# Kernel tuning notes

Measured on AMD Instinct MI355X. Metric: run time of the kernel, lower is better.

Reference implementation:

```python
import jax, jax.numpy as jnp
import numpy as np

N = 50000      # nodes
E = 800000     # edges
IN = 128       # in_channels
H = 128        # hidden_channels
OUT = 40       # out_channels (classes)
EPS = 1e-5     # LayerNorm eps


def _glorot(key, fan_in, fan_out):
    lim = np.sqrt(6.0 / (fan_in + fan_out)).astype(np.float32)
    return jax.random.uniform(key, (fan_in, fan_out), jnp.float32, -lim, lim)


def setup_inputs() -> dict:
    key = jax.random.key(0)
    ks = jax.random.split(key, 8)
    x = jax.random.normal(ks[0], (N, IN), jnp.float32)
    edge_index = jax.random.randint(ks[1], (2, E), 0, N, jnp.int32)
    return {
        "x": x,
        "W0": _glorot(ks[2], IN, H), "b0": jnp.zeros((H,), jnp.float32),
        "W1": _glorot(ks[3], H, H),  "b1": jnp.zeros((H,), jnp.float32),
        "W2": _glorot(ks[4], H, OUT), "b2": jnp.zeros((OUT,), jnp.float32),
        "ln1_g": jnp.ones((H,), jnp.float32), "ln1_b": jnp.zeros((H,), jnp.float32),
        "ln2_g": jnp.ones((H,), jnp.float32), "ln2_b": jnp.zeros((H,), jnp.float32),
        "edge_index": edge_index,
    }


def reference(x, W0, b0, W1, b1, W2, b2, ln1_g, ln1_b, ln2_g, ln2_b, edge_index):
    # GCN normalization with self-loops: A_hat = D^-1/2 (A + I) D^-1/2
    self_idx = jnp.arange(N, dtype=edge_index.dtype)
    src = jnp.concatenate([edge_index[0], self_idx])  # [E+N]
    dst = jnp.concatenate([edge_index[1], self_idx])
    deg = jax.ops.segment_sum(jnp.ones_like(src, jnp.float32), dst, num_segments=N)
    dinv = jax.lax.rsqrt(deg)  # deg >= 1 thanks to self-loops
    norm = dinv[src] * dinv[dst]  # [E+N]

    def conv(h, W, b):
        h = h @ W                                  # [N, F] dense GEMM
        msg = h[src] * norm[:, None]               # gather + scale [E+N, F]
        return jax.ops.segment_sum(msg, dst, num_segments=N) + b

    def layernorm(h, g, b):
        mu = jnp.mean(h, axis=-1, keepdims=True)
        var = jnp.mean(jnp.square(h - mu), axis=-1, keepdims=True)
        return (h - mu) * jax.lax.rsqrt(var + EPS) * g + b

    # layer 0 (note: original uses lns[i+1], so lns[0] is never applied)
    h = jax.nn.relu(layernorm(conv(x, W0, b0), ln1_g, ln1_b))
    # dropout is identity in eval mode
    h = jax.nn.relu(layernorm(conv(h, W1, b1), ln2_g, ln2_b))
    h = conv(h, W2, b2)
    return jax.nn.log_softmax(h, axis=-1)
```

## Files before the change

### kernel.cpp

```cpp
#include <hip/hip_runtime.h>
#include <math.h>

typedef __attribute__((ext_vector_type(8))) short bf16x8;
typedef __attribute__((ext_vector_type(4))) float f32x4;
typedef unsigned short u16;
typedef unsigned int u32;

static __device__ __forceinline__ u16 f2bf(float f) {
    unsigned u = __float_as_uint(f);
    unsigned r = (u + 0x7fff + ((u >> 16) & 1)) >> 16;
    return (u16)r;
}
static __device__ __forceinline__ float bf2f(u16 h) {
    return __uint_as_float(((unsigned)h) << 16);
}
static __device__ __forceinline__ float pk_lo(u32 u) { return __uint_as_float(u << 16); }
static __device__ __forceinline__ float pk_hi(u32 u) { return __uint_as_float(u & 0xffff0000u); }

__global__ void init_k(int* __restrict__ counts, int n, int gN,
                       const float* __restrict__ W0, const float* __restrict__ W1,
                       const float* __restrict__ W2,
                       u16* __restrict__ w0hi, u16* __restrict__ w0lo,
                       u16* __restrict__ w1hi, u16* __restrict__ w1lo,
                       u16* __restrict__ w2hi, u16* __restrict__ w2lo) {
    int b = blockIdx.x;
    if (b < gN) {
        int i = b * 256 + threadIdx.x;
        if (i < n) counts[i] = 0;
        return;
    }
    int i = (b - gN) * 256 + threadIdx.x;
    const float* W; u16 *hi, *lo; int COLS, cin, idx;
    if (i < 16384)      { W = W0; hi = w0hi; lo = w0lo; COLS = 128; cin = 128; idx = i; }
    else if (i < 32768) { W = W1; hi = w1hi; lo = w1lo; COLS = 128; cin = 128; idx = i - 16384; }
    else if (i < 40960) { W = W2; hi = w2hi; lo = w2lo; COLS = 64;  cin = 40;  idx = i - 32768; }
    else return;
    int k = idx / COLS, col = idx % COLS;
    float v = (col < cin) ? W[k * cin + col] : 0.f;
    u16 h = f2bf(v);
    u16 l = f2bf(v - bf2f(h));
    int ct = col >> 4, ks = k >> 5, ln = (col & 15) + (((k >> 3) & 3) << 4), j = k & 7;
    int pos = (((ct * 4 + ks) * 64 + ln) << 3) + j;
    hi[pos] = h; lo[pos] = l;
}

__global__ void count_rank_k(const int* __restrict__ dst, int* __restrict__ counts,
                             u16* __restrict__ rank, int e) {
    int i = blockIdx.x * 256 + threadIdx.x;
    if (i < e) rank[i] = (u16)atomicAdd(&counts[dst[i]], 1);
}
__global__ __launch_bounds__(1024) void scan1_k(const int* __restrict__ counts,
                                                int* __restrict__ offs,
                                                int* __restrict__ bsum,
                                                float* __restrict__ dinv, int n) {
    __shared__ int ws[16];
    int tid = threadIdx.x;
    int i = blockIdx.x * 1024 + tid;
    int lane = tid & 63, w = tid >> 6;
    int c = (i < n) ? counts[i] : 0;
    if (i < n) dinv[i] = rsqrtf((float)c + 1.0f);
    int s = c;
#pragma unroll
    for (int o = 1; o < 64; o <<= 1) { int t = __shfl_up(s, o); if (lane >= o) s += t; }
    if (lane == 63) ws[w] = s;
    __syncthreads();
    if (w == 0) {
        int x = (lane < 16) ? ws[lane] : 0;
#pragma unroll
        for (int o = 1; o < 16; o <<= 1) { int t = __shfl_up(x, o); if (lane >= o) x += t; }
        if (lane < 16) ws[lane] = x;
    }
    __syncthreads();
    int base = (w > 0) ? ws[w - 1] : 0;
    int incl = base + s;
    if (i < n) offs[i + 1] = incl;
    if (tid == 1023) bsum[blockIdx.x] = incl;
}
__global__ void scan23_k(int* __restrict__ offs, const int* __restrict__ bsum,
                         int nb, int n) {
    __shared__ int pre[64];
    int tid = threadIdx.x;
    if (tid < 64) {
        int v = (tid < nb) ? bsum[tid] : 0;
#pragma unroll
        for (int o = 1; o < 64; o <<= 1) { int t = __shfl_up(v, o); if (tid >= o) v += t; }
        pre[tid] = v;
    }
    __syncthreads();
    int i = blockIdx.x * 256 + tid;
    if (i == 0) offs[0] = 0;
    if (i < n) {
        int b = i >> 10;
        offs[i + 1] += (b > 0) ? pre[b - 1] : 0;
    }
}

__global__ __launch_bounds__(256) void fill_gemm1_k(const int* __restrict__ src,
                                                    const int* __restrict__ dst,
                                                    const u16* __restrict__ rank,
                                                    const int* __restrict__ offs,
                                                    u16* __restrict__ csr, int e, int fillBlocks,
                                                    const float* __restrict__ A,
                                                    const u16* __restrict__ Whi,
                                                    const u16* __restrict__ Wlo,
                                                    const float* __restrict__ dinv,
                                                    u16* __restrict__ C, int nrows) {
    if ((int)blockIdx.x < fillBlocks) {
        int i = blockIdx.x * 256 + threadIdx.x;
        if (i < e) csr[offs[dst[i]] + (int)rank[i]] = (u16)src[i];
        return;
    }
    constexpr int COLS = 128;
    int bid = blockIdx.x - fillBlocks;
    int wave = threadIdx.x >> 6, lane = threadIdx.x & 63;
    int r0 = bid * 64 + wave * 16;
    int arow = min(r0 + (lane & 15), nrows - 1);
    int kbase = (lane >> 4) * 8;

    bf16x8 ahi[4], alo[4];
#pragma unroll
    for (int ks = 0; ks < 4; ++ks) {
        const float* ap = &A[(long)arow * 128 + ks * 32 + kbase];
        float4 f0 = *(const float4*)ap;
        float4 f1 = *(const float4*)(ap + 4);
        float fv[8] = {f0.x, f0.y, f0.z, f0.w, f1.x, f1.y, f1.z, f1.w};
#pragma unroll
        for (int j = 0; j < 8; ++j) {
            u16 h = f2bf(fv[j]);
            ahi[ks][j] = (short)h;
            alo[ks][j] = (short)f2bf(fv[j] - bf2f(h));
        }
    }
    float dscale[4];
#pragma unroll
    for (int r = 0; r < 4; ++r) {
        int orow = r0 + (lane >> 4) * 4 + r;
        dscale[r] = (orow < nrows) ? dinv[orow] : 0.f;
    }
#pragma unroll
    for (int ct = 0; ct < COLS / 16; ct += 2) {
        f32x4 acc0 = {0.f, 0.f, 0.f, 0.f}, acc1 = {0.f, 0.f, 0.f, 0.f};
#pragma unroll
        for (int ks = 0; ks < 4; ++ks) {
            int fo0 = ((ct * 4 + ks) * 64 + lane) * 8;
            int fo1 = (((ct + 1) * 4 + ks) * 64 + lane) * 8;
            bf16x8 bhi0 = *(const bf16x8*)&Whi[fo0];
            bf16x8 blo0 = *(const bf16x8*)&Wlo[fo0];
            bf16x8 bhi1 = *(const bf16x8*)&Whi[fo1];
            bf16x8 blo1 = *(const bf16x8*)&Wlo[fo1];
            acc0 = __builtin_amdgcn_mfma_f32_16x16x32_bf16(ahi[ks], bhi0, acc0, 0, 0, 0);
            acc1 = __builtin_amdgcn_mfma_f32_16x16x32_bf16(ahi[ks], bhi1, acc1, 0, 0, 0);
            acc0 = __builtin_amdgcn_mfma_f32_16x16x32_bf16(alo[ks], bhi0, acc0, 0, 0, 0);
            acc1 = __builtin_amdgcn_mfma_f32_16x16x32_bf16(alo[ks], bhi1, acc1, 0, 0, 0);
            acc0 = __builtin_amdgcn_mfma_f32_16x16x32_bf16(ahi[ks], blo0, acc0, 0, 0, 0);
            acc1 = __builtin_amdgcn_mfma_f32_16x16x32_bf16(ahi[ks], blo1, acc1, 0, 0, 0);
        }
#pragma unroll
        for (int r = 0; r < 4; ++r) {
            int orow = r0 + (lane >> 4) * 4 + r;
            if (orow < nrows) {
                C[(long)orow * COLS + ct * 16 + (lane & 15)] = f2bf(acc0[r] * dscale[r]);
                C[(long)orow * COLS + (ct + 1) * 16 + (lane & 15)] = f2bf(acc1[r] * dscale[r]);
            }
        }
    }
}

template<int COLS>
__global__ __launch_bounds__(256) void mfma_gemm_bf16a_k(const u16* __restrict__ A,
                                                         const u16* __restrict__ Whi,
                                                         const u16* __restrict__ Wlo,
                                                         const float* __restrict__ dinv,
                                                         u16* __restrict__ C, int nrows) {
    int wave = threadIdx.x >> 6, lane = threadIdx.x & 63;
    int r0 = blockIdx.x * 64 + wave * 16;
    int arow = min(r0 + (lane & 15), nrows - 1);
    int kbase = (lane >> 4) * 8;

    bf16x8 a[4];
#pragma unroll
    for (int ks = 0; ks < 4; ++ks)
        a[ks] = *(const bf16x8*)&A[(long)arow * 128 + ks * 32 + kbase];

    float dscale[4];
#pragma unroll
    for (int r = 0; r < 4; ++r) {
        int orow = r0 + (lane >> 4) * 4 + r;
        dscale[r] = (orow < nrows) ? dinv[orow] : 0.f;
    }
#pragma unroll
    for (int ct = 0; ct < COLS / 16; ct += 2) {
        f32x4 acc0 = {0.f, 0.f, 0.f, 0.f}, acc1 = {0.f, 0.f, 0.f, 0.f};
#pragma unroll
        for (int ks = 0; ks < 4; ++ks) {
            int fo0 = ((ct * 4 + ks) * 64 + lane) * 8;
            int fo1 = (((ct + 1) * 4 + ks) * 64 + lane) * 8;
            bf16x8 bhi0 = *(const bf16x8*)&Whi[fo0];
            bf16x8 blo0 = *(const bf16x8*)&Wlo[fo0];
            bf16x8 bhi1 = *(const bf16x8*)&Whi[fo1];
            bf16x8 blo1 = *(const bf16x8*)&Wlo[fo1];
            acc0 = __builtin_amdgcn_mfma_f32_16x16x32_bf16(a[ks], bhi0, acc0, 0, 0, 0);
            acc1 = __builtin_amdgcn_mfma_f32_16x16x32_bf16(a[ks], bhi1, acc1, 0, 0, 0);
            acc0 = __builtin_amdgcn_mfma_f32_16x16x32_bf16(a[ks], blo0, acc0, 0, 0, 0);
            acc1 = __builtin_amdgcn_mfma_f32_16x16x32_bf16(a[ks], blo1, acc1, 0, 0, 0);
        }
#pragma unroll
        for (int r = 0; r < 4; ++r) {
            int orow = r0 + (lane >> 4) * 4 + r;
            if (orow < nrows) {
                C[(long)orow * COLS + ct * 16 + (lane & 15)] = f2bf(acc0[r] * dscale[r]);
                C[(long)orow * COLS + (ct + 1) * 16 + (lane & 15)] = f2bf(acc1[r] * dscale[r]);
            }
        }
    }
}

__global__ __launch_bounds__(256) void agg_ln_relu_k(const u16* __restrict__ Cs,
                                                     const int* __restrict__ offs,
                                                     const u16* __restrict__ csr,
                                                     const float* __restrict__ dinv,
                                                     const float* __restrict__ bias,
                                                     const float* __restrict__ g,
                                                     const float* __restrict__ b,
                                                     u16* __restrict__ out, int n) {
    int wid = (blockIdx.x * 256 + threadIdx.x) >> 6;
    int lane = threadIdx.x & 63;
    if (wid >= n) return;
    const u32* C2 = (const u32*)Cs;
    u32 su = C2[(long)wid * 64 + lane];
    float ax = pk_lo(su), ay = pk_hi(su), bx2 = 0.f, by2 = 0.f;
    int beg = offs[wid], end = offs[wid + 1];
    int j = beg;
    while (j < end) {
        int take = min(64, end - j);
        int myidx = (lane < take) ? (int)csr[j + lane] : 0;
        int k = 0;
        for (; k + 8 <= take; k += 8) {
            int i0 = __shfl(myidx, k),     i1 = __shfl(myidx, k + 1);
            int i2 = __shfl(myidx, k + 2), i3 = __shfl(myidx, k + 3);
            int i4 = __shfl(myidx, k + 4), i5 = __shfl(myidx, k + 5);
            int i6 = __shfl(myidx, k + 6), i7 = __shfl(myidx, k + 7);
            u32 u0 = C2[(long)i0 * 64 + lane], u1 = C2[(long)i1 * 64 + lane];
            u32 u2 = C2[(long)i2 * 64 + lane], u3 = C2[(long)i3 * 64 + lane];
            u32 u4 = C2[(long)i4 * 64 + lane], u5 = C2[(long)i5 * 64 + lane];
            u32 u6 = C2[(long)i6 * 64 + lane], u7 = C2[(long)i7 * 64 + lane];
            ax += pk_lo(u0) + pk_lo(u1) + pk_lo(u2) + pk_lo(u3);
            ay += pk_hi(u0) + pk_hi(u1) + pk_hi(u2) + pk_hi(u3);
            bx2 += pk_lo(u4) + pk_lo(u5) + pk_lo(u6) + pk_lo(u7);
            by2 += pk_hi(u4) + pk_hi(u5) + pk_hi(u6) + pk_hi(u7);
        }
        for (; k < take; ++k) {
            int i0 = __shfl(myidx, k);
            u32 u0 = C2[(long)i0 * 64 + lane];
            ax += pk_lo(u0); ay += pk_hi(u0);
        }
        j += take;
    }
    float w = dinv[wid];
    float2 bia = ((const float2*)bias)[lane];
    float t0 = (ax + bx2) * w + bia.x;
    float t1 = (ay + by2) * w + bia.y;
    float s = t0 + t1;
#pragma unroll
    for (int off = 32; off; off >>= 1) s += __shfl_xor(s, off);
    float mu = s * (1.f / 128.f);
    float d0 = t0 - mu, d1 = t1 - mu;
    float v = d0 * d0 + d1 * d1;
#pragma unroll
    for (int off = 32; off; off >>= 1) v += __shfl_xor(v, off);
    float rstd = rsqrtf(v * (1.f / 128.f) + 1e-5f);
    float2 gv = ((const float2*)g)[lane];
    float2 bv = ((const float2*)b)[lane];
    float y0 = fmaxf(0.f, d0 * rstd * gv.x + bv.x);
    float y1 = fmaxf(0.f, d1 * rstd * gv.y + bv.y);
    ((u32*)out)[(long)wid * 64 + lane] = ((u32)f2bf(y1) << 16) | f2bf(y0);
}

__global__ __launch_bounds__(256) void agg_lsm_k(const u16* __restrict__ Cs,
                                                 const int* __restrict__ offs,
                                                 const u16* __restrict__ csr,
                                                 const float* __restrict__ dinv,
                                                 const float* __restrict__ b2,
                                                 float* __restrict__ out, int n) {
    int wid = (blockIdx.x * 256 + threadIdx.x) >> 6;
    int lane = threadIdx.x & 63;
    if (wid >= n) return;
    float aa = bf2f(Cs[(long)wid * 64 + lane]), ab = 0.f;
    int beg = offs[wid], end = offs[wid + 1];
    int j = beg;
    while (j < end) {
        int take = min(64, end - j);
        int myidx = (lane < take) ? (int)csr[j + lane] : 0;
        int k = 0;
        for (; k + 8 <= take; k += 8) {
            int i0 = __shfl(myidx, k),     i1 = __shfl(myidx, k + 1);
            int i2 = __shfl(myidx, k + 2), i3 = __shfl(myidx, k + 3);
            int i4 = __shfl(myidx, k + 4), i5 = __shfl(myidx, k + 5);
            int i6 = __shfl(myidx, k + 6), i7 = __shfl(myidx, k + 7);
            float v0 = bf2f(Cs[(long)i0 * 64 + lane]), v1 = bf2f(Cs[(long)i1 * 64 + lane]);
            float v2 = bf2f(Cs[(long)i2 * 64 + lane]), v3 = bf2f(Cs[(long)i3 * 64 + lane]);
            float v4 = bf2f(Cs[(long)i4 * 64 + lane]), v5 = bf2f(Cs[(long)i5 * 64 + lane]);
            float v6 = bf2f(Cs[(long)i6 * 64 + lane]), v7 = bf2f(Cs[(long)i7 * 64 + lane]);
            aa += v0 + v1 + v2 + v3;
            ab += v4 + v5 + v6 + v7;
        }
        for (; k < take; ++k) {
            int i0 = __shfl(myidx, k);
            aa += bf2f(Cs[(long)i0 * 64 + lane]);
        }
        j += take;
    }
    float v = (lane < 40) ? (aa + ab) * dinv[wid] + b2[lane] : -INFINITY;
    float m = v;
#pragma unroll
    for (int off = 32; off; off >>= 1) m = fmaxf(m, __shfl_xor(m, off));
    float e = (lane < 40) ? expf(v - m) : 0.f;
    float s = e;
#pragma unroll
    for (int off = 32; off; off >>= 1) s += __shfl_xor(s, off);
    float r = v - m - logf(s);
    if (lane < 40) out[(long)wid * 40 + lane] = r;
}

extern "C" void kernel_launch(void* const* d_in, const int* in_sizes, int n_in,
                              void* d_out, int out_size, void* d_ws, size_t ws_size,
                              hipStream_t stream) {
    const float* x    = (const float*)d_in[0];
    const float* W0   = (const float*)d_in[1];
    const float* b0   = (const float*)d_in[2];
    const float* W1   = (const float*)d_in[3];
    const float* b1   = (const float*)d_in[4];
    const float* W2   = (const float*)d_in[5];
    const float* b2   = (const float*)d_in[6];
    const float* ln1g = (const float*)d_in[7];
    const float* ln1b = (const float*)d_in[8];
    const float* ln2g = (const float*)d_in[9];
    const float* ln2b = (const float*)d_in[10];
    const int*   ei   = (const int*)d_in[11];

    const int N = in_sizes[0] / 128;
    const int E = in_sizes[11] / 2;
    const int* esrc = ei;
    const int* edst = ei + E;
    float* out = (float*)d_out;

    const int Npad = ((N + 255) / 256) * 256;

    int* counts  = (int*)d_ws;
    int* offs    = counts + Npad;
    int* bsum    = offs + Npad;
    u16* rank16  = (u16*)(bsum + 64);
    u16* csr16   = rank16 + E;
    float* dinv  = (float*)(csr16 + E);
    u16* bufA    = (u16*)(dinv + Npad);
    u16* bufB    = bufA + (size_t)N * 128;
    u16* w0hi    = bufB + (size_t)N * 128;
    u16* w0lo    = w0hi + 16384;
    u16* w1hi    = w0lo + 16384;
    u16* w1lo    = w1hi + 16384;
    u16* w2hi    = w1lo + 16384;
    u16* w2lo    = w2hi + 8192;

    dim3 blk(256);
    int gN = (N + 255) / 256, gE = (E + 255) / 256;
    int nb1024 = (N + 1023) / 1024;
    int gG = (N + 63) / 64;
    int gW = (N + 3) / 4;

    init_k<<<gN + 160, blk, 0, stream>>>(counts, N, gN, W0, W1, W2,
                                         w0hi, w0lo, w1hi, w1lo, w2hi, w2lo);
    count_rank_k<<<gE, blk, 0, stream>>>(edst, counts, rank16, E);
    scan1_k<<<nb1024, 1024, 0, stream>>>(counts, offs, bsum, dinv, N);
    scan23_k<<<gN, blk, 0, stream>>>(offs, bsum, nb1024, N);
    fill_gemm1_k<<<gE + gG, blk, 0, stream>>>(esrc, edst, rank16, offs, csr16, E, gE,
                                              x, w0hi, w0lo, dinv, bufA, N);
    agg_ln_relu_k<<<gW, blk, 0, stream>>>(bufA, offs, csr16, dinv, b0, ln1g, ln1b, bufB, N);
    mfma_gemm_bf16a_k<128><<<gG, blk, 0, stream>>>(bufB, w1hi, w1lo, dinv, bufA, N);
    agg_ln_relu_k<<<gW, blk, 0, stream>>>(bufA, offs, csr16, dinv, b1, ln2g, ln2b, bufB, N);
    mfma_gemm_bf16a_k<64><<<gG, blk, 0, stream>>>(bufB, w2hi, w2lo, dinv, bufA, N);
    agg_lsm_k<<<gW, blk, 0, stream>>>(bufA, offs, csr16, dinv, b2, out, N);
}
```

Baseline: 207.1 us.

## Split wavefront across multiple edges per iteration with vectorized row loads in aggregation

After: 211.7 us. 1.02x slower.

```diff
diff --git a/kernel.cpp b/kernel.cpp
--- a/kernel.cpp
+++ b/kernel.cpp
@@ -227,53 +227,66 @@
     int lane = threadIdx.x & 63;
     if (wid >= n) return;
     const u32* C2 = (const u32*)Cs;
-    u32 su = C2[(long)wid * 64 + lane];
-    float ax = pk_lo(su), ay = pk_hi(su), bx2 = 0.f, by2 = 0.f;
+    int half = lane >> 5;
+    int w = lane & 31;
+    float a0 = 0.f, a1 = 0.f, a2 = 0.f, a3 = 0.f;
+    float c0 = 0.f, c1 = 0.f, c2 = 0.f, c3 = 0.f;
+    if (half == 0) {
+        uint2 u = *(const uint2*)&C2[(size_t)wid * 64 + 2 * w];
+        a0 = pk_lo(u.x); a1 = pk_hi(u.x); a2 = pk_lo(u.y); a3 = pk_hi(u.y);
+    }
     int beg = offs[wid], end = offs[wid + 1];
-    int j = beg;
-    while (j < end) {
+    for (int j = beg; j < end; j += 64) {
         int take = min(64, end - j);
         int myidx = (lane < take) ? (int)csr[j + lane] : 0;
         int k = 0;
-        for (; k + 8 <= take; k += 8) {
-            int i0 = __shfl(myidx, k),     i1 = __shfl(myidx, k + 1);
-            int i2 = __shfl(myidx, k + 2), i3 = __shfl(myidx, k + 3);
-            int i4 = __shfl(myidx, k + 4), i5 = __shfl(myidx, k + 5);
-            int i6 = __shfl(myidx, k + 6), i7 = __shfl(myidx, k + 7);
-            u32 u0 = C2[(long)i0 * 64 + lane], u1 = C2[(long)i1 * 64 + lane];
-            u32 u2 = C2[(long)i2 * 64 + lane], u3 = C2[(long)i3 * 64 + lane];
-            u32 u4 = C2[(long)i4 * 64 + lane], u5 = C2[(long)i5 * 64 + lane];
-            u32 u6 = C2[(long)i6 * 64 + lane], u7 = C2[(long)i7 * 64 + lane];
-            ax += pk_lo(u0) + pk_lo(u1) + pk_lo(u2) + pk_lo(u3);
-            ay += pk_hi(u0) + pk_hi(u1) + pk_hi(u2) + pk_hi(u3);
-            bx2 += pk_lo(u4) + pk_lo(u5) + pk_lo(u6) + pk_lo(u7);
-            by2 += pk_hi(u4) + pk_hi(u5) + pk_hi(u6) + pk_hi(u7);
-        }
-        for (; k < take; ++k) {
-            int i0 = __shfl(myidx, k);
-            u32 u0 = C2[(long)i0 * 64 + lane];
-            ax += pk_lo(u0); ay += pk_hi(u0);
-        }
-        j += take;
-    }
-    float w = dinv[wid];
-    float2 bia = ((const float2*)bias)[lane];
-    float t0 = (ax + bx2) * w + bia.x;
-    float t1 = (ay + by2) * w + bia.y;
-    float s = t0 + t1;
-#pragma unroll
-    for (int off = 32; off; off >>= 1) s += __shfl_xor(s, off);
-    float mu = s * (1.f / 128.f);
-    float d0 = t0 - mu, d1 = t1 - mu;
-    float v = d0 * d0 + d1 * d1;
-#pragma unroll
-    for (int off = 32; off; off >>= 1) v += __shfl_xor(v, off);
-    float rstd = rsqrtf(v * (1.f / 128.f) + 1e-5f);
-    float2 gv = ((const float2*)g)[lane];
-    float2 bv = ((const float2*)b)[lane];
+        for (; k + 16 <= take; k += 16) {
+#pragma unroll
+            for (int it = 0; it < 8; ++it) {
+                int s = __shfl(myidx, k + it * 2 + half);
+                uint2 u = *(const uint2*)&C2[(size_t)s * 64 + 2 * w];
+                if (it & 1) { c0 += pk_lo(u.x); c1 += pk_hi(u.x); c2 += pk_lo(u.y); c3 += pk_hi(u.y); }
+                else        { a0 += pk_lo(u.x); a1 += pk_hi(u.x); a2 += pk_lo(u.y); a3 += pk_hi(u.y); }
+            }
+        }
+        for (; k < take; k += 2) {
+            int e = k + half;
+            bool v = e < take;
+            int s = __shfl(myidx, v ? e : 0);
+            if (v) {
+                uint2 u = *(const uint2*)&C2[(size_t)s * 64 + 2 * w];
+                a0 += pk_lo(u.x); a1 += pk_hi(u.x); a2 += pk_lo(u.y); a3 += pk_hi(u.y);
+            }
+        }
+    }
+    a0 += c0; a1 += c1; a2 += c2; a3 += c3;
+    a0 += __shfl_xor(a0, 32); a1 += __shfl_xor(a1, 32);
+    a2 += __shfl_xor(a2, 32); a3 += __shfl_xor(a3, 32);
+    float dv = dinv[wid];
+    float4 bi = ((const float4*)bias)[w];
+    float t0 = a0 * dv + bi.x, t1 = a1 * dv + bi.y;
+    float t2 = a2 * dv + bi.z, t3 = a3 * dv + bi.w;
+    float s4 = t0 + t1 + t2 + t3;
+#pragma unroll
+    for (int o = 1; o < 32; o <<= 1) s4 += __shfl_xor(s4, o);
+    float mu = s4 * (1.f / 128.f);
+    float d0 = t0 - mu, d1 = t1 - mu, d2 = t2 - mu, d3 = t3 - mu;
+    float q = d0 * d0 + d1 * d1 + d2 * d2 + d3 * d3;
+#pragma unroll
+    for (int o = 1; o < 32; o <<= 1) q += __shfl_xor(q, o);
+    float rstd = rsqrtf(q * (1.f / 128.f) + 1e-5f);
+    float4 gv = ((const float4*)g)[w];
+    float4 bv = ((const float4*)b)[w];
     float y0 = fmaxf(0.f, d0 * rstd * gv.x + bv.x);
     float y1 = fmaxf(0.f, d1 * rstd * gv.y + bv.y);
-    ((u32*)out)[(long)wid * 64 + lane] = ((u32)f2bf(y1) << 16) | f2bf(y0);
+    float y2 = fmaxf(0.f, d2 * rstd * gv.z + bv.z);
+    float y3 = fmaxf(0.f, d3 * rstd * gv.w + bv.w);
+    if (half == 0) {
+        uint2 o2;
+        o2.x = ((u32)f2bf(y1) << 16) | f2bf(y0);
+        o2.y = ((u32)f2bf(y3) << 16) | f2bf(y2);
+        *(uint2*)&((u32*)out)[(size_t)wid * 64 + 2 * w] = o2;
+    }
 }
 
 __global__ __launch_bounds__(256) void agg_lsm_k(const u16* __restrict__ Cs,
@@ -285,41 +298,64 @@
     int wid = (blockIdx.x * 256 + threadIdx.x) >> 6;
     int lane = threadIdx.x & 63;
     if (wid >= n) return;
-    float aa = bf2f(Cs[(long)wid * 64 + lane]), ab = 0.f;
+    const u32* C2 = (const u32*)Cs;
+    int slot = lane >> 4;
+    int w = lane & 15;
+    float a0 = 0.f, a1 = 0.f, a2 = 0.f, a3 = 0.f;
+    float c0 = 0.f, c1 = 0.f, c2 = 0.f, c3 = 0.f;
+    if (slot == 0) {
+        uint2 u = *(const uint2*)&C2[(size_t)wid * 32 + 2 * w];
+        a0 = pk_lo(u.x); a1 = pk_hi(u.x); a2 = pk_lo(u.y); a3 = pk_hi(u.y);
+    }
     int beg = offs[wid], end = offs[wid + 1];
-    int j = beg;
-    while (j < end) {
+    for (int j = beg; j < end; j += 64) {
         int take = min(64, end - j);
         int myidx = (lane < take) ? (int)csr[j + lane] : 0;
         int k = 0;
-        for (; k + 8 <= take; k += 8) {
-            int i0 = __shfl(myidx, k),     i1 = __shfl(myidx, k + 1);
-            int i2 = __shfl(myidx, k + 2), i3 = __shfl(myidx, k + 3);
-            int i4 = __shfl(myidx, k + 4), i5 = __shfl(myidx, k + 5);
-            int i6 = __shfl(myidx, k + 6), i7 = __shfl(myidx, k + 7);
-            float v0 = bf2f(Cs[(long)i0 * 64 + lane]), v1 = bf2f(Cs[(long)i1 * 64 + lane]);
-            float v2 = bf2f(Cs[(long)i2 * 64 + lane]), v3 = bf2f(Cs[(long)i3 * 64 + lane]);
-            float v4 = bf2f(Cs[(long)i4 * 64 + lane]), v5 = bf2f(Cs[(long)i5 * 64 + lane]);
-            float v6 = bf2f(Cs[(long)i6 * 64 + lane]), v7 = bf2f(Cs[(long)i7 * 64 + lane]);
-            aa += v0 + v1 + v2 + v3;
-            ab += v4 + v5 + v6 + v7;
-        }
-        for (; k < take; ++k) {
-            int i0 = __shfl(myidx, k);
-            aa += bf2f(Cs[(long)i0 * 64 + lane]);
-        }
-        j += take;
-    }
-    float v = (lane < 40) ? (aa + ab) * dinv[wid] + b2[lane] : -INFINITY;
-    float m = v;
-#pragma unroll
-    for (int off = 32; off; off >>= 1) m = fmaxf(m, __shfl_xor(m, off));
-    float e = (lane < 40) ? expf(v - m) : 0.f;
-    float s = e;
-#pragma unroll
-    for (int off = 32; off; off >>= 1) s += __shfl_xor(s, off);
-    float r = v - m - logf(s);
-    if (lane < 40) out[(long)wid * 40 + lane] = r;
+        for (; k + 16 <= take; k += 16) {
+#pragma unroll
+            for (int it = 0; it < 4; ++it) {
+                int s = __shfl(myidx, k + it * 4 + slot);
+                uint2 u = *(const uint2*)&C2[(size_t)s * 32 + 2 * w];
+                if (it & 1) { c0 += pk_lo(u.x); c1 += pk_hi(u.x); c2 += pk_lo(u.y); c3 += pk_hi(u.y); }
+                else        { a0 += pk_lo(u.x); a1 += pk_hi(u.x); a2 += pk_lo(u.y); a3 += pk_hi(u.y); }
+            }
+        }
+        for (; k < take; k += 4) {
+            int e = k + slot;
+            bool v = e < take;
+            int s = __shfl(myidx, v ? e : 0);
+            if (v) {
+                uint2 u = *(const uint2*)&C2[(size_t)s * 32 + 2 * w];
+                a0 += pk_lo(u.x); a1 += pk_hi(u.x); a2 += pk_lo(u.y); a3 += pk_hi(u.y);
+            }
+        }
+    }
+    a0 += c0; a1 += c1; a2 += c2; a3 += c3;
+#pragma unroll
+    for (int m2 = 16; m2 < 64; m2 <<= 1) {
+        a0 += __shfl_xor(a0, m2); a1 += __shfl_xor(a1, m2);
+        a2 += __shfl_xor(a2, m2); a3 += __shfl_xor(a3, m2);
+    }
+    float dv = dinv[wid];
+    float v0 = -INFINITY, v1 = -INFINITY, v2 = -INFINITY, v3 = -INFINITY;
+    if (w < 10) {
+        float4 bb = ((const float4*)b2)[w];
+        v0 = a0 * dv + bb.x; v1 = a1 * dv + bb.y;
+        v2 = a2 * dv + bb.z; v3 = a3 * dv + bb.w;
+    }
+    float m = fmaxf(fmaxf(v0, v1), fmaxf(v2, v3));
+#pragma unroll
+    for (int o = 1; o < 16; o <<= 1) m = fmaxf(m, __shfl_xor(m, o));
+    float es = 0.f;
+    if (w < 10) es = expf(v0 - m) + expf(v1 - m) + expf(v2 - m) + expf(v3 - m);
+#pragma unroll
+    for (int o = 1; o < 16; o <<= 1) es += __shfl_xor(es, o);
+    float ls = logf(es);
+    if (slot == 0 && w < 10) {
+        float4 r = make_float4(v0 - m - ls, v1 - m - ls, v2 - m - ls, v3 - m - ls);
+        *(float4*)&out[(size_t)wid * 40 + 4 * w] = r;
+    }
 }
 
 extern "C" void kernel_launch(void* const* d_in, const int* in_sizes, int n_in,
```

## Overlap GEMM with edge counting and split aggregation/GEMM into node halves

Applied to the files above, without the earlier changes.

After: 205.7 us, median of 2. About the same (-0.7%).

```diff
diff --git a/kernel.cpp b/kernel.cpp
--- a/kernel.cpp
+++ b/kernel.cpp
@@ -44,74 +44,11 @@
     hi[pos] = h; lo[pos] = l;
 }
 
-__global__ void count_rank_k(const int* __restrict__ dst, int* __restrict__ counts,
-                             u16* __restrict__ rank, int e) {
-    int i = blockIdx.x * 256 + threadIdx.x;
-    if (i < e) rank[i] = (u16)atomicAdd(&counts[dst[i]], 1);
-}
-__global__ __launch_bounds__(1024) void scan1_k(const int* __restrict__ counts,
-                                                int* __restrict__ offs,
-                                                int* __restrict__ bsum,
-                                                float* __restrict__ dinv, int n) {
-    __shared__ int ws[16];
-    int tid = threadIdx.x;
-    int i = blockIdx.x * 1024 + tid;
-    int lane = tid & 63, w = tid >> 6;
-    int c = (i < n) ? counts[i] : 0;
-    if (i < n) dinv[i] = rsqrtf((float)c + 1.0f);
-    int s = c;
-#pragma unroll
-    for (int o = 1; o < 64; o <<= 1) { int t = __shfl_up(s, o); if (lane >= o) s += t; }
-    if (lane == 63) ws[w] = s;
-    __syncthreads();
-    if (w == 0) {
-        int x = (lane < 16) ? ws[lane] : 0;
-#pragma unroll
-        for (int o = 1; o < 16; o <<= 1) { int t = __shfl_up(x, o); if (lane >= o) x += t; }
-        if (lane < 16) ws[lane] = x;
-    }
-    __syncthreads();
-    int base = (w > 0) ? ws[w - 1] : 0;
-    int incl = base + s;
-    if (i < n) offs[i + 1] = incl;
-    if (tid == 1023) bsum[blockIdx.x] = incl;
-}
-__global__ void scan23_k(int* __restrict__ offs, const int* __restrict__ bsum,
-                         int nb, int n) {
-    __shared__ int pre[64];
-    int tid = threadIdx.x;
-    if (tid < 64) {
-        int v = (tid < nb) ? bsum[tid] : 0;
-#pragma unroll
-        for (int o = 1; o < 64; o <<= 1) { int t = __shfl_up(v, o); if (tid >= o) v += t; }
-        pre[tid] = v;
-    }
-    __syncthreads();
-    int i = blockIdx.x * 256 + tid;
-    if (i == 0) offs[0] = 0;
-    if (i < n) {
-        int b = i >> 10;
-        offs[i + 1] += (b > 0) ? pre[b - 1] : 0;
-    }
-}
-
-__global__ __launch_bounds__(256) void fill_gemm1_k(const int* __restrict__ src,
-                                                    const int* __restrict__ dst,
-                                                    const u16* __restrict__ rank,
-                                                    const int* __restrict__ offs,
-                                                    u16* __restrict__ csr, int e, int fillBlocks,
-                                                    const float* __restrict__ A,
-                                                    const u16* __restrict__ Whi,
-                                                    const u16* __restrict__ Wlo,
-                                                    const float* __restrict__ dinv,
-                                                    u16* __restrict__ C, int nrows) {
-    if ((int)blockIdx.x < fillBlocks) {
-        int i = blockIdx.x * 256 + threadIdx.x;
-        if (i < e) csr[offs[dst[i]] + (int)rank[i]] = (u16)src[i];
-        return;
-    }
+static __device__ __forceinline__ void gemm1_body(int bid, const float* __restrict__ A,
+                                                  const u16* __restrict__ Whi,
+                                                  const u16* __restrict__ Wlo,
+                                                  u16* __restrict__ C, int nrows) {
     constexpr int COLS = 128;
-    int bid = blockIdx.x - fillBlocks;
     int wave = threadIdx.x >> 6, lane = threadIdx.x & 63;
     int r0 = bid * 64 + wave * 16;
     int arow = min(r0 + (lane & 15), nrows - 1);
@@ -130,12 +67,6 @@
             ahi[ks][j] = (short)h;
             alo[ks][j] = (short)f2bf(fv[j] - bf2f(h));
         }
-    }
-    float dscale[4];
-#pragma unroll
-    for (int r = 0; r < 4; ++r) {
-        int orow = r0 + (lane >> 4) * 4 + r;
-        dscale[r] = (orow < nrows) ? dinv[orow] : 0.f;
     }
 #pragma unroll
     for (int ct = 0; ct < COLS / 16; ct += 2) {
@@ -159,22 +90,111 @@
         for (int r = 0; r < 4; ++r) {
             int orow = r0 + (lane >> 4) * 4 + r;
             if (orow < nrows) {
-                C[(long)orow * COLS + ct * 16 + (lane & 15)] = f2bf(acc0[r] * dscale[r]);
-                C[(long)orow * COLS + (ct + 1) * 16 + (lane & 15)] = f2bf(acc1[r] * dscale[r]);
+                C[(long)orow * COLS + ct * 16 + (lane & 15)] = f2bf(acc0[r]);
+                C[(long)orow * COLS + (ct + 1) * 16 + (lane & 15)] = f2bf(acc1[r]);
             }
         }
     }
 }
 
+__global__ __launch_bounds__(256) void cg1_k(const int* __restrict__ dst,
+                                             int* __restrict__ counts,
+                                             u16* __restrict__ rank, int e,
+                                             const float* __restrict__ A,
+                                             const u16* __restrict__ Whi,
+                                             const u16* __restrict__ Wlo,
+                                             u16* __restrict__ C, int nrows, int gemmBlocks) {
+    int bid = blockIdx.x;
+    int k = bid / 5, r = bid % 5;
+    if (r == 4) {
+        if (k < gemmBlocks) gemm1_body(k, A, Whi, Wlo, C, nrows);
+        return;
+    }
+    int i = (k * 4 + r) * 256 + threadIdx.x;
+    if (i < e) rank[i] = (u16)atomicAdd(&counts[dst[i]], 1);
+}
+
+__global__ __launch_bounds__(1024) void scan1_k(const int* __restrict__ counts,
+                                                int* __restrict__ offs,
+                                                int* __restrict__ bsum,
+                                                float* __restrict__ dinv, int n) {
+    __shared__ int ws[16];
+    int tid = threadIdx.x;
+    int i = blockIdx.x * 1024 + tid;
+    int lane = tid & 63, w = tid >> 6;
+    int c = (i < n) ? counts[i] : 0;
+    if (i < n) dinv[i] = rsqrtf((float)c + 1.0f);
+    int s = c;
+#pragma unroll
+    for (int o = 1; o < 64; o <<= 1) { int t = __shfl_up(s, o); if (lane >= o) s += t; }
+    if (lane == 63) ws[w] = s;
+    __syncthreads();
+    if (w == 0) {
+        int x = (lane < 16) ? ws[lane] : 0;
+#pragma unroll
+        for (int o = 1; o < 16; o <<= 1) { int t = __shfl_up(x, o); if (lane >= o) x += t; }
+        if (lane < 16) ws[lane] = x;
+    }
+    __syncthreads();
+    int base = (w > 0) ? ws[w - 1] : 0;
+    int incl = base + s;
+    if (i < n) offs[i + 1] = incl;
+    if (tid == 1023) bsum[blockIdx.x] = incl;
+}
+__global__ void scan23_k(int* __restrict__ offs, const int* __restrict__ bsum,
+                         int nb, int n) {
+    __shared__ int pre[64];
+    int tid = threadIdx.x;
+    if (tid < 64) {
+        int v = (tid < nb) ? bsum[tid] : 0;
+#pragma unroll
+        for (int o = 1; o < 64; o <<= 1) { int t = __shfl_up(v, o); if (tid >= o) v += t; }
+        pre[tid] = v;
+    }
+    __syncthreads();
+    int i = blockIdx.x * 256 + tid;
+    if (i == 0) offs[0] = 0;
+    if (i < n) {
+        int b = i >> 10;
+        offs[i + 1] += (b > 0) ? pre[b - 1] : 0;
+    }
+}
+
+__global__ __launch_bounds__(256) void fr_k(const int* __restrict__ src,
+                                            const int* __restrict__ dst,
+                                            const u16* __restrict__ rank,
+                                            const int* __restrict__ offs,
+                                            u16* __restrict__ csr, int e,
+                                            u16* __restrict__ Cs,
+                                            const float* __restrict__ dinv, int n) {
+    int bid = blockIdx.x;
+    int k = bid / 3, r = bid % 3;
+    if (r == 2) {
+        int i = k * 256 + threadIdx.x;
+        if (i < e) csr[offs[dst[i]] + (int)rank[i]] = (u16)src[i];
+        return;
+    }
+    int t = (k * 2 + r) * 256 + threadIdx.x;
+    if (t >= n * 32) return;
+    int row = t >> 5;
+    float w = dinv[row];
+    uint2 u = ((uint2*)Cs)[t];
+    uint2 o2;
+    o2.x = ((u32)f2bf(pk_hi(u.x) * w) << 16) | f2bf(pk_lo(u.x) * w);
+    o2.y = ((u32)f2bf(pk_hi(u.y) * w) << 16) | f2bf(pk_lo(u.y) * w);
+    ((uint2*)Cs)[t] = o2;
+}
+
 template<int COLS>
-__global__ __launch_bounds__(256) void mfma_gemm_bf16a_k(const u16* __restrict__ A,
-                                                         const u16* __restrict__ Whi,
-                                                         const u16* __restrict__ Wlo,
-                                                         const float* __restrict__ dinv,
-                                                         u16* __restrict__ C, int nrows) {
+static __device__ __forceinline__ void gemm_body(int bid, const u16* __restrict__ A,
+                                                 const u16* __restrict__ Whi,
+                                                 const u16* __restrict__ Wlo,
+                                                 const float* __restrict__ dinv,
+                                                 u16* __restrict__ C, int rowOff, int rowEnd) {
     int wave = threadIdx.x >> 6, lane = threadIdx.x & 63;
-    int r0 = blockIdx.x * 64 + wave * 16;
-    int arow = min(r0 + (lane & 15), nrows - 1);
+    int r0 = rowOff + bid * 64 + wave * 16;
+    if (r0 >= rowEnd) return;
+    int arow = min(r0 + (lane & 15), rowEnd - 1);
     int kbase = (lane >> 4) * 8;
 
     bf16x8 a[4];
@@ -186,7 +206,7 @@
 #pragma unroll
     for (int r = 0; r < 4; ++r) {
         int orow = r0 + (lane >> 4) * 4 + r;
-        dscale[r] = (orow < nrows) ? dinv[orow] : 0.f;
+        dscale[r] = (orow < rowEnd) ? dinv[orow] : 0.f;
     }
 #pragma unroll
     for (int ct = 0; ct < COLS / 16; ct += 2) {
@@ -207,7 +227,7 @@
 #pragma unroll
         for (int r = 0; r < 4; ++r) {
             int orow = r0 + (lane >> 4) * 4 + r;
-            if (orow < nrows) {
+            if (orow < rowEnd) {
                 C[(long)orow * COLS + ct * 16 + (lane & 15)] = f2bf(acc0[r] * dscale[r]);
                 C[(long)orow * COLS + (ct + 1) * 16 + (lane & 15)] = f2bf(acc1[r] * dscale[r]);
             }
@@ -215,17 +235,15 @@
     }
 }
 
-__global__ __launch_bounds__(256) void agg_ln_relu_k(const u16* __restrict__ Cs,
-                                                     const int* __restrict__ offs,
-                                                     const u16* __restrict__ csr,
-                                                     const float* __restrict__ dinv,
-                                                     const float* __restrict__ bias,
-                                                     const float* __restrict__ g,
-                                                     const float* __restrict__ b,
-                                                     u16* __restrict__ out, int n) {
-    int wid = (blockIdx.x * 256 + threadIdx.x) >> 6;
-    int lane = threadIdx.x & 63;
-    if (wid >= n) return;
+static __device__ __forceinline__ void agg_ln_body(int wid, int lane,
+                                                   const u16* __restrict__ Cs,
+                                                   const int* __restrict__ offs,
+                                                   const u16* __restrict__ csr,
+                                                   const float* __restrict__ dinv,
+                                                   const float* __restrict__ bias,
+                                                   const float* __restrict__ g,
+                                                   const float* __restrict__ b,
+                                                   u16* __restrict__ out) {
     const u32* C2 = (const u32*)Cs;
     u32 su = C2[(long)wid * 64 + lane];
     float ax = pk_lo(su), ay = pk_hi(su), bx2 = 0.f, by2 = 0.f;
@@ -274,6 +292,57 @@
     float y0 = fmaxf(0.f, d0 * rstd * gv.x + bv.x);
     float y1 = fmaxf(0.f, d1 * rstd * gv.y + bv.y);
     ((u32*)out)[(long)wid * 64 + lane] = ((u32)f2bf(y1) << 16) | f2bf(y0);
+}
+
+__global__ __launch_bounds__(256) void agg_half_k(const u16* __restrict__ Cs,
+                                                  const int* __restrict__ offs,
+                                                  const u16* __restrict__ csr,
+                                                  const float* __restrict__ dinv,
+                                                  const float* __restrict__ bias,
+                                                  const float* __restrict__ g,
+                                                  const float* __restrict__ b,
+                                                  u16* __restrict__ out,
+                                                  int nodeOff, int nodeEnd) {
+    int wid = nodeOff + ((blockIdx.x * 256 + threadIdx.x) >> 6);
+    int lane = threadIdx.x & 63;
+    if (wid >= nodeEnd) return;
+    agg_ln_body(wid, lane, Cs, offs, csr, dinv, bias, g, b, out);
+}
+
+template<int COLS>
+__global__ __launch_bounds__(256) void aggemm_k(const u16* __restrict__ CsAgg,
+                                                const int* __restrict__ offs,
+                                                const u16* __restrict__ csr,
+                                                const float* __restrict__ dinv,
+                                                const float* __restrict__ bias,
+                                                const float* __restrict__ g,
+                                                const float* __restrict__ b,
+                                                u16* __restrict__ hOut,
+                                                int nodeOff, int nodeEnd,
+                                                const u16* __restrict__ A,
+                                                const u16* __restrict__ Whi,
+                                                const u16* __restrict__ Wlo,
+                                                u16* __restrict__ C, int rowEnd, int gemmBlocks) {
+    int bid = blockIdx.x;
+    int k = bid / 17, r = bid % 17;
+    if (r == 16) {
+        if (k < gemmBlocks) gemm_body<COLS>(k, A, Whi, Wlo, dinv, C, 0, rowEnd);
+        return;
+    }
+    int aggIdx = k * 16 + r;
+    int wid = nodeOff + ((aggIdx * 256 + (int)threadIdx.x) >> 6);
+    int lane = threadIdx.x & 63;
+    if (wid >= nodeEnd) return;
+    agg_ln_body(wid, lane, CsAgg, offs, csr, dinv, bias, g, b, hOut);
+}
+
+template<int COLS>
+__global__ __launch_bounds__(256) void gemm_half_k(const u16* __restrict__ A,
+                                                   const u16* __restrict__ Whi,
+                                                   const u16* __restrict__ Wlo,
+                                                   const float* __restrict__ dinv,
+                                                   u16* __restrict__ C, int rowOff, int rowEnd) {
+    gemm_body<COLS>(blockIdx.x, A, Whi, Wlo, dinv, C, rowOff, rowEnd);
 }
 
 __global__ __launch_bounds__(256) void agg_lsm_k(const u16* __restrict__ Cs,
@@ -345,6 +414,7 @@
     float* out = (float*)d_out;
 
     const int Npad = ((N + 255) / 256) * 256;
+    const int N2 = N / 2;
 
     int* counts  = (int*)d_ws;
     int* offs    = counts + Npad;
@@ -354,7 +424,8 @@
     float* dinv  = (float*)(csr16 + E);
     u16* bufA    = (u16*)(dinv + Npad);
     u16* bufB    = bufA + (size_t)N * 128;
-    u16* w0hi    = bufB + (size_t)N * 128;
+    u16* bufC    = bufB + (size_t)N * 128;
+    u16* w0hi    = bufC + (size_t)N * 128;
     u16* w0lo    = w0hi + 16384;
     u16* w1hi    = w0lo + 16384;
     u16* w1lo    = w1hi + 16384;
@@ -362,21 +433,28 @@
     u16* w2lo    = w2hi + 8192;
 
     dim3 blk(256);
-    int gN = (N + 255) / 256, gE = (E + 255) / 256;
+    int gN = (N + 255) / 256;
+    int gE = (E + 255) / 256;
     int nb1024 = (N + 1023) / 1024;
     int gG = (N + 63) / 64;
+    int gGh = (N2 + 63) / 64;
+    int gAh = (N2 + 3) / 4;
     int gW = (N + 3) / 4;
 
     init_k<<<gN + 160, blk, 0, stream>>>(counts, N, gN, W0, W1, W2,
                                          w0hi, w0lo, w1hi, w1lo, w2hi, w2lo);
-    count_rank_k<<<gE, blk, 0, stream>>>(edst, counts, rank16, E);
+    cg1_k<<<5 * gG, blk, 0, stream>>>(edst, counts, rank16, E,
+                                      x, w0hi, w0lo, bufA, N, gG);
     scan1_k<<<nb1024, 1024, 0, stream>>>(counts, offs, bsum, dinv, N);
     scan23_k<<<gN, blk, 0, stream>>>(offs, bsum, nb1024, N);
-    fill_gemm1_k<<<gE + gG, blk, 0, stream>>>(esrc, edst, rank16, offs, csr16, E, gE,
-                                              x, w0hi, w0lo, dinv, bufA, N);
-    agg_ln_relu_k<<<gW, blk, 0, stream>>>(bufA, offs, csr16, dinv, b0, ln1g, ln1b, bufB, N);
-    mfma_gemm_bf16a_k<128><<<gG, blk, 0, stream>>>(bufB, w1hi, w1lo, dinv, bufA, N);
-    agg_ln_relu_k<<<gW, blk, 0, stream>>>(bufA, offs, csr16, dinv, b1, ln2g, ln2b, bufB, N);
-    mfma_gemm_bf16a_k<64><<<gG, blk, 0, stream>>>(bufB, w2hi, w2lo, dinv, bufA, N);
-    agg_lsm_k<<<gW, blk, 0, stream>>>(bufA, offs, csr16, dinv, b2, out, N);
-}
+    fr_k<<<3 * gE, blk, 0, stream>>>(esrc, edst, rank16, offs, csr16, E, bufA, dinv, N);
+    agg_half_k<<<gAh, blk, 0, stream>>>(bufA, offs, csr16, dinv, b0, ln1g, ln1b, bufB, 0, N2);
+    aggemm_k<128><<<17 * gGh, blk, 0, stream>>>(bufA, offs, csr16, dinv, b0, ln1g, ln1b, bufB,
+                                                N2, N, bufB, w1hi, w1lo, bufC, N2, gGh);
+    gemm_half_k<128><<<gGh, blk, 0, stream>>>(bufB, w1hi, w1lo, dinv, bufC, N2, N);
+    agg_half_k<<<gAh, blk, 0, stream>>>(bufC, offs, csr16, dinv, b1, ln2g, ln2b, bufA, 0, N2);
+    aggemm_k<64><<<17 * gGh, blk, 0, stream>>>(bufC, offs, csr16, dinv, b1, ln2g, ln2b, bufA,
+                                               N2, N, bufA, w2hi, w2lo, bufB, N2, gGh);
+    gemm_half_k<64><<<gGh, blk, 0, stream>>>(bufA, w2hi, w2lo, dinv, bufB, N2, N);
+    agg_lsm_k<<<gW, blk, 0, stream>>>(bufB, offs, csr16, dinv, b2, out, N);
+}
```
